# Optimization experiments

Measured on AMD Instinct MI355X. Metric: run time of the kernel, lower is better.

## Reference

```python
import jax, jax.numpy as jnp
import numpy as np

IS_CAUSAL = True
NEG_INF = float('-inf')


def setup_inputs() -> dict:
    key = jax.random.key(0)
    kq, kk, kv = jax.random.split(key, 3)
    B, H, S, D = 4, 16, 2048, 64
    return {
        'query': jax.random.normal(kq, (B, H, S, D), dtype=jnp.float32),
        'key': jax.random.normal(kk, (B, H, S, D), dtype=jnp.float32),
        'value': jax.random.normal(kv, (B, H, S, D), dtype=jnp.float32),
    }


def reference(query, key, value):
    # Attention(Q,K,V) = softmax(QK^T / sqrt(d_k) + causal_mask) V
    d_k = query.shape[-1]
    scale = 1.0 / np.sqrt(d_k).astype(np.float32)
    # [B,H,Sq,Sk]
    scores = jnp.einsum('bhqd,bhkd->bhqk', query, key) * scale
    if IS_CAUSAL:
        sq, sk = query.shape[-2], key.shape[-2]
        causal = jnp.triu(jnp.ones((sq, sk), dtype=bool), k=1)
        scores = jnp.where(causal[None, None, :, :], NEG_INF, scores)
    weights = jax.nn.softmax(scores, axis=-1)
    # dropout p=0.0 (eval): identity
    out = jnp.einsum('bhqk,bhkd->bhqd', weights, value)
    return out
```

## Files before the change

### kernel.cpp

```cpp
#include <hip/hip_runtime.h>
#include <stdint.h>


#define SLEN 2048
#define DHEAD 64
#define NHEADS 64
#define NELEM (SLEN * DHEAD * NHEADS)
#define PADP 72
#define OMPAD 68

typedef short bf16x8 __attribute__((ext_vector_type(8)));
typedef float f32x4 __attribute__((ext_vector_type(4)));

__device__ __forceinline__ uint32_t pkbf(float hi, float lo) {
    uint32_t a = __builtin_bit_cast(uint32_t, lo) + 0x8000u;
    uint32_t b = __builtin_bit_cast(uint32_t, hi) + 0x8000u;
    return __builtin_amdgcn_perm(b, a, 0x07060302u);
}
__device__ __forceinline__ unsigned short f2bf(float f) {
    return (unsigned short)((__builtin_bit_cast(uint32_t, f) + 0x8000u) >> 16);
}

__global__ __launch_bounds__(256)
void convert_prep(const float* __restrict__ K, const float* __restrict__ V,
                  unsigned short* __restrict__ Kb, unsigned short* __restrict__ Vtb) {
    __shared__ unsigned short Lt[64 * 264];
    const int b = blockIdx.x, t = threadIdx.x;
    if (b < 4096) {
        const int off = (b * 256 + t) * 8;
        float4 a = *(const float4*)(K + off);
        float4 c = *(const float4*)(K + off + 4);
        uint4 o;
        o.x = pkbf(a.y, a.x); o.y = pkbf(a.w, a.z);
        o.z = pkbf(c.y, c.x); o.w = pkbf(c.w, c.z);
        *(uint4*)(Kb + off) = o;
    } else {
        const int vb2 = b - 4096;
        const int head = vb2 >> 3, kblk = vb2 & 7;
        const float* Vh = V + (size_t)head * (SLEN * DHEAD) + kblk * 256 * DHEAD;
        unsigned short* Vo = Vtb + (size_t)head * (SLEN * DHEAD) + kblk * 256;
#pragma unroll
        for (int i = 0; i < 16; ++i) {
            int idx = t + 256 * i;
            int key = idx >> 4, d4 = idx & 15;
            float4 v = *(const float4*)(Vh + key * DHEAD + d4 * 4);
            Lt[(d4 * 4 + 0) * 264 + key] = f2bf(v.x);
            Lt[(d4 * 4 + 1) * 264 + key] = f2bf(v.y);
            Lt[(d4 * 4 + 2) * 264 + key] = f2bf(v.z);
            Lt[(d4 * 4 + 3) * 264 + key] = f2bf(v.w);
        }
        __syncthreads();
#pragma unroll
        for (int jj = 0; jj < 8; ++jj) {
            int idx = t + 256 * jj;
            int d = idx >> 5, k8 = idx & 31;
            *(uint4*)(Vo + (size_t)d * SLEN + k8 * 8) = *(const uint4*)(Lt + d * 264 + k8 * 8);
        }
    }
}

__global__ __launch_bounds__(128, 2)
void sdpa_mfma(const float* __restrict__ Qf, const unsigned short* __restrict__ Kb,
               const unsigned short* __restrict__ Vtb, float* __restrict__ Og) {
    const int n    = blockIdx.x;
    const int head = n & 63;
    const int A    = n >> 6;
    const int TB   = 31 - A;

    const size_t hb = (size_t)head * SLEN * DHEAD;
    const float* Qh = Qf + hb;
    const unsigned short* Kh  = Kb + hb;
    const unsigned short* Vth = Vtb + hb;
    float* Oh = Og + hb;

    const int tid  = threadIdx.x;
    const int w    = tid >> 6, lane = tid & 63;
    const int cl   = lane & 15, quad = lane >> 4;

    __shared__ unsigned short Pl[2 * 64 * PADP];
    __shared__ float Om[64 * OMPAD];
    __shared__ float Lsm[64];

    unsigned short* Plw = Pl + w * 64 * PADP;
    const float SCL = 0.18033688f;

    bf16x8 qf[4][2];
    bf16x8 kbn[4][2];
    f32x4  o[4][4];
    float  ls[4];

    auto load_qf = [&](int qw) {
#pragma unroll
        for (int m = 0; m < 4; ++m)
#pragma unroll
            for (int h = 0; h < 2; ++h) {
                const float* src = Qh + (size_t)(qw + m * 16 + cl) * DHEAD + h * 32 + quad * 8;
                float4 a = *(const float4*)src;
                float4 b = *(const float4*)(src + 4);
                uint4 u;
                u.x = pkbf(a.y * SCL, a.x * SCL); u.y = pkbf(a.w * SCL, a.z * SCL);
                u.z = pkbf(b.y * SCL, b.x * SCL); u.w = pkbf(b.w * SCL, b.z * SCL);
                qf[m][h] = __builtin_bit_cast(bf16x8, u);
            }
    };
    auto zero_acc = [&]() {
#pragma unroll
        for (int m = 0; m < 4; ++m) {
            ls[m] = 0.f;
#pragma unroll
            for (int d = 0; d < 4; ++d) o[m][d] = (f32x4){0.f, 0.f, 0.f, 0.f};
        }
    };
    auto load_kb = [&](int j, bf16x8 kb[4][2]) {
        const unsigned short* base = Kh + (size_t)j * 64 * DHEAD;
#pragma unroll
        for (int kk = 0; kk < 4; ++kk)
#pragma unroll
            for (int h = 0; h < 2; ++h)
                kb[kk][h] = __builtin_bit_cast(bf16x8,
                    *(const uint4*)(base + (kk * 16 + cl) * DHEAD + h * 32 + quad * 8));
    };

    auto do_steps = [&](int tq, int js, int je) {
        if (js >= je) return;
        load_kb(js, kbn);
        for (int j = js; j < je; ++j) {
            bf16x8 vb[4][2];
            const unsigned short* vbase = Vth + j * 64;
#pragma unroll
            for (int dd = 0; dd < 4; ++dd)
#pragma unroll
                for (int h = 0; h < 2; ++h)
                    vb[dd][h] = __builtin_bit_cast(bf16x8,
                        *(const uint4*)(vbase + (size_t)(dd * 16 + cl) * SLEN + h * 32 + quad * 8));

            const bool partial = (j == tq);
#pragma unroll
            for (int kk = 0; kk < 4; ++kk) {
                const int krel = kk * 16 + quad * 4;
#pragma unroll
                for (int qq = 0; qq < 4; ++qq) {
                    f32x4 s = (f32x4){0.f, 0.f, 0.f, 0.f};
                    s = __builtin_amdgcn_mfma_f32_16x16x32_bf16(kbn[kk][0], qf[qq][0], s, 0, 0, 0);
                    s = __builtin_amdgcn_mfma_f32_16x16x32_bf16(kbn[kk][1], qf[qq][1], s, 0, 0, 0);
                    float p0, p1, p2, p3;
                    if (partial) {
                        const int qrel = qq * 16 + cl;
                        p0 = (krel + 0 <= qrel) ? __builtin_amdgcn_exp2f(s[0]) : 0.f;
                        p1 = (krel + 1 <= qrel) ? __builtin_amdgcn_exp2f(s[1]) : 0.f;
                        p2 = (krel + 2 <= qrel) ? __builtin_amdgcn_exp2f(s[2]) : 0.f;
                        p3 = (krel + 3 <= qrel) ? __builtin_amdgcn_exp2f(s[3]) : 0.f;
                    } else {
                        p0 = __builtin_amdgcn_exp2f(s[0]);
                        p1 = __builtin_amdgcn_exp2f(s[1]);
                        p2 = __builtin_amdgcn_exp2f(s[2]);
                        p3 = __builtin_amdgcn_exp2f(s[3]);
                    }
                    ls[qq] += (p0 + p1) + (p2 + p3);
                    uint2 pw;
                    pw.x = pkbf(p1, p0);
                    pw.y = pkbf(p3, p2);
                    *(uint2*)(Plw + (qq * 16 + cl) * PADP + kk * 16 + quad * 4) = pw;
                }
            }
            const int jn = (j + 1 < je) ? j + 1 : j;
            load_kb(jn, kbn);

            bf16x8 pa[4][2];
#pragma unroll
            for (int m = 0; m < 4; ++m)
#pragma unroll
                for (int h = 0; h < 2; ++h)
                    pa[m][h] = __builtin_bit_cast(bf16x8,
                        *(const uint4*)(Plw + (m * 16 + cl) * PADP + h * 32 + quad * 8));
#pragma unroll
            for (int m = 0; m < 4; ++m)
#pragma unroll
                for (int dd = 0; dd < 4; ++dd) {
                    o[m][dd] = __builtin_amdgcn_mfma_f32_16x16x32_bf16(pa[m][0], vb[dd][0], o[m][dd], 0, 0, 0);
                    o[m][dd] = __builtin_amdgcn_mfma_f32_16x16x32_bf16(pa[m][1], vb[dd][1], o[m][dd], 0, 0, 0);
                }
        }
    };
    auto reduce_ls = [&]() {
#pragma unroll
        for (int qq = 0; qq < 4; ++qq) {
            float v = ls[qq];
            v += __shfl_xor(v, 16);
            v += __shfl_xor(v, 32);
            ls[qq] = v;
        }
    };
    auto store_tile = [&](int qw, const float lsr[4]) {
#pragma unroll
        for (int m = 0; m < 4; ++m)
#pragma unroll
            for (int r = 0; r < 4; ++r) {
                const float inv = 1.0f / __shfl(lsr[m], quad * 4 + r);
#pragma unroll
                for (int dd = 0; dd < 4; ++dd)
                    Oh[(size_t)(qw + m * 16 + quad * 4 + r) * DHEAD + dd * 16 + cl] = o[m][dd][r] * inv;
            }
    };

    if (w == 0) {
        load_qf(A * 64);
        zero_acc();
        do_steps(A, 0, A + 1);
        reduce_ls();
        store_tile(A * 64, ls);
        load_qf(TB * 64);
        zero_acc();
        do_steps(TB, 0, 16 - A);
        reduce_ls();
    } else {
        load_qf(TB * 64);
        zero_acc();
        do_steps(TB, 16 - A, 32 - A);
        reduce_ls();
    }

    if (w == 1) {
#pragma unroll
        for (int m = 0; m < 4; ++m)
#pragma unroll
            for (int dd = 0; dd < 4; ++dd)
                *(f32x4*)(Om + (dd * 16 + cl) * OMPAD + m * 16 + quad * 4) = o[m][dd];
        if (quad == 0) {
#pragma unroll
            for (int qq = 0; qq < 4; ++qq) Lsm[qq * 16 + cl] = ls[qq];
        }
    }
    __syncthreads();
    if (w == 0) {
#pragma unroll
        for (int m = 0; m < 4; ++m)
#pragma unroll
            for (int dd = 0; dd < 4; ++dd)
                o[m][dd] += *(const f32x4*)(Om + (dd * 16 + cl) * OMPAD + m * 16 + quad * 4);
        float lc[4];
#pragma unroll
        for (int qq = 0; qq < 4; ++qq) lc[qq] = ls[qq] + Lsm[qq * 16 + cl];
        store_tile(TB * 64, lc);
    }
}

extern "C" void kernel_launch(void* const* d_in, const int* in_sizes, int n_in,
                              void* d_out, int out_size, void* d_ws, size_t ws_size,
                              hipStream_t stream) {
    const float* Q = (const float*)d_in[0];
    const float* K = (const float*)d_in[1];
    const float* V = (const float*)d_in[2];
    float*       O = (float*)d_out;

    unsigned short* Kbf  = (unsigned short*)d_ws;
    unsigned short* Vtbf = Kbf + NELEM;

    convert_prep<<<dim3(4096 + 512), dim3(256), 0, stream>>>(K, V, Kbf, Vtbf);
    sdpa_mfma<<<dim3(1024), dim3(128), 0, stream>>>(Q, Kbf, Vtbf, O);
}
```

Before: 205.2 us.

## Shrink query tiles to 32 rows and pass P through bpermute instead of LDS

Query tiles shrink from 64 to 32 rows, so each block now runs four waves, as two pairs that each balance a light and a heavy causal tile. This raises occupancy, with launch bounds of 256 threads and 4 blocks. The probability tile is no longer written to and re-read from shared memory; it is rearranged into the MFMA A-operand layout with ds_bpermute in registers. The K-tile prefetch across iterations is dropped, and each wave now loads the same K/V for only half as many query rows, which lowers reuse per load.

```diff
diff --git a/kernel.cpp b/kernel.cpp
--- a/kernel.cpp
+++ b/kernel.cpp
@@ -6,8 +6,6 @@
 #define DHEAD 64
 #define NHEADS 64
 #define NELEM (SLEN * DHEAD * NHEADS)
-#define PADP 72
-#define OMPAD 68
 
 typedef short bf16x8 __attribute__((ext_vector_type(8)));
 typedef float f32x4 __attribute__((ext_vector_type(4)));
@@ -59,42 +57,44 @@
     }
 }
 
-__global__ __launch_bounds__(128, 2)
+__global__ __launch_bounds__(256, 4)
 void sdpa_mfma(const float* __restrict__ Qf, const unsigned short* __restrict__ Kb,
                const unsigned short* __restrict__ Vtb, float* __restrict__ Og) {
-    const int n    = blockIdx.x;
+    const int n = blockIdx.x;
     const int head = n & 63;
-    const int A    = n >> 6;
-    const int TB   = 31 - A;
+    const int cp = n >> 6;
+    const int tid = threadIdx.x;
+    const int w = tid >> 6, lane = tid & 63;
+    const int cl = lane & 15, quad = lane >> 4;
+    const int ch = w >> 1, role = w & 1;
+    const int c = cp + 16 * ch;
+    const int subA = c, subB = 63 - c;
+    const int Sa = (c >> 1) + 1;
+    const int Sb = ((63 - c) >> 1) + 1;
 
     const size_t hb = (size_t)head * SLEN * DHEAD;
     const float* Qh = Qf + hb;
-    const unsigned short* Kh  = Kb + hb;
+    const unsigned short* Kh = Kb + hb;
     const unsigned short* Vth = Vtb + hb;
     float* Oh = Og + hb;
 
-    const int tid  = threadIdx.x;
-    const int w    = tid >> 6, lane = tid & 63;
-    const int cl   = lane & 15, quad = lane >> 4;
-
-    __shared__ unsigned short Pl[2 * 64 * PADP];
-    __shared__ float Om[64 * OMPAD];
-    __shared__ float Lsm[64];
-
-    unsigned short* Plw = Pl + w * 64 * PADP;
+    __shared__ float Om[2][64 * 36];
+    __shared__ float Lsm[2][32];
+
+    const int idx0 = 4 * (cl + 32 * (quad & 1));
+    const int idx1 = idx0 + 64;
     const float SCL = 0.18033688f;
 
-    bf16x8 qf[4][2];
-    bf16x8 kbn[4][2];
-    f32x4  o[4][4];
-    float  ls[4];
-
-    auto load_qf = [&](int qw) {
-#pragma unroll
-        for (int m = 0; m < 4; ++m)
+    bf16x8 qf[2][2];
+    f32x4 o[2][4];
+    float ls[2];
+
+    auto load_qf = [&](int i) {
+#pragma unroll
+        for (int m = 0; m < 2; ++m)
 #pragma unroll
             for (int h = 0; h < 2; ++h) {
-                const float* src = Qh + (size_t)(qw + m * 16 + cl) * DHEAD + h * 32 + quad * 8;
+                const float* src = Qh + (size_t)(i * 32 + m * 16 + cl) * DHEAD + h * 32 + quad * 8;
                 float4 a = *(const float4*)src;
                 float4 b = *(const float4*)(src + 4);
                 uint4 u;
@@ -105,47 +105,45 @@
     };
     auto zero_acc = [&]() {
 #pragma unroll
-        for (int m = 0; m < 4; ++m) {
+        for (int m = 0; m < 2; ++m) {
             ls[m] = 0.f;
 #pragma unroll
             for (int d = 0; d < 4; ++d) o[m][d] = (f32x4){0.f, 0.f, 0.f, 0.f};
         }
     };
-    auto load_kb = [&](int j, bf16x8 kb[4][2]) {
-        const unsigned short* base = Kh + (size_t)j * 64 * DHEAD;
-#pragma unroll
-        for (int kk = 0; kk < 4; ++kk)
-#pragma unroll
-            for (int h = 0; h < 2; ++h)
-                kb[kk][h] = __builtin_bit_cast(bf16x8,
-                    *(const uint4*)(base + (kk * 16 + cl) * DHEAD + h * 32 + quad * 8));
-    };
-
-    auto do_steps = [&](int tq, int js, int je) {
-        if (js >= je) return;
-        load_kb(js, kbn);
+
+    auto do_steps = [&](int i, int js, int je) {
+        const int jd = i >> 1;
+        const int qrb = 32 * (i & 1);
         for (int j = js; j < je; ++j) {
-            bf16x8 vb[4][2];
+            const unsigned short* kbase = Kh + (size_t)j * 64 * DHEAD;
+            bf16x8 kb[4][2];
+#pragma unroll
+            for (int kk = 0; kk < 4; ++kk)
+#pragma unroll
+                for (int h = 0; h < 2; ++h)
+                    kb[kk][h] = __builtin_bit_cast(bf16x8,
+                        *(const uint4*)(kbase + (kk * 16 + cl) * DHEAD + h * 32 + quad * 8));
             const unsigned short* vbase = Vth + j * 64;
-#pragma unroll
-            for (int dd = 0; dd < 4; ++dd)
-#pragma unroll
-                for (int h = 0; h < 2; ++h)
-                    vb[dd][h] = __builtin_bit_cast(bf16x8,
-                        *(const uint4*)(vbase + (size_t)(dd * 16 + cl) * SLEN + h * 32 + quad * 8));
-
-            const bool partial = (j == tq);
+            bf16x8 vb0[4];
+#pragma unroll
+            for (int dd = 0; dd < 4; ++dd)
+                vb0[dd] = __builtin_bit_cast(bf16x8,
+                    *(const uint4*)(vbase + (size_t)(dd * 16 + cl) * SLEN + quad * 8));
+
+            uint32_t Sd[2][4][2];
+            const bool partial = (j == jd);
 #pragma unroll
             for (int kk = 0; kk < 4; ++kk) {
                 const int krel = kk * 16 + quad * 4;
 #pragma unroll
-                for (int qq = 0; qq < 4; ++qq) {
+                for (int qq = 0; qq < 2; ++qq) {
                     f32x4 s = (f32x4){0.f, 0.f, 0.f, 0.f};
-                    s = __builtin_amdgcn_mfma_f32_16x16x32_bf16(kbn[kk][0], qf[qq][0], s, 0, 0, 0);
-                    s = __builtin_amdgcn_mfma_f32_16x16x32_bf16(kbn[kk][1], qf[qq][1], s, 0, 0, 0);
+                    s = __builtin_amdgcn_mfma_f32_16x16x32_bf16(kb[kk][0], qf[qq][0], s, 0, 0, 0);
+                    s = __builtin_amdgcn_mfma_f32_16x16x32_bf16(kb[kk][1], qf[qq][1], s, 0, 0, 0);
                     float p0, p1, p2, p3;
                     if (partial) {
-                        const int qrel = qq * 16 + cl;
+                        const int qrel = qrb + qq * 16 + cl;
                         p0 = (krel + 0 <= qrel) ? __builtin_amdgcn_exp2f(s[0]) : 0.f;
                         p1 = (krel + 1 <= qrel) ? __builtin_amdgcn_exp2f(s[1]) : 0.f;
                         p2 = (krel + 2 <= qrel) ? __builtin_amdgcn_exp2f(s[2]) : 0.f;
@@ -157,91 +155,95 @@
                         p3 = __builtin_amdgcn_exp2f(s[3]);
                     }
                     ls[qq] += (p0 + p1) + (p2 + p3);
-                    uint2 pw;
-                    pw.x = pkbf(p1, p0);
-                    pw.y = pkbf(p3, p2);
-                    *(uint2*)(Plw + (qq * 16 + cl) * PADP + kk * 16 + quad * 4) = pw;
+                    Sd[qq][kk][0] = pkbf(p1, p0);
+                    Sd[qq][kk][1] = pkbf(p3, p2);
                 }
             }
-            const int jn = (j + 1 < je) ? j + 1 : j;
-            load_kb(jn, kbn);
-
-            bf16x8 pa[4][2];
-#pragma unroll
-            for (int m = 0; m < 4; ++m)
-#pragma unroll
-                for (int h = 0; h < 2; ++h)
-                    pa[m][h] = __builtin_bit_cast(bf16x8,
-                        *(const uint4*)(Plw + (m * 16 + cl) * PADP + h * 32 + quad * 8));
-#pragma unroll
-            for (int m = 0; m < 4; ++m)
+            bf16x8 vb1[4];
+#pragma unroll
+            for (int dd = 0; dd < 4; ++dd)
+                vb1[dd] = __builtin_bit_cast(bf16x8,
+                    *(const uint4*)(vbase + (size_t)(dd * 16 + cl) * SLEN + 32 + quad * 8));
+
+            bf16x8 pa[2][2];
+#pragma unroll
+            for (int qq = 0; qq < 2; ++qq)
+#pragma unroll
+                for (int h = 0; h < 2; ++h) {
+                    uint32_t dw[4];
+#pragma unroll
+                    for (int dp = 0; dp < 4; ++dp) {
+                        const int id = (dp < 2) ? idx0 : idx1;
+                        int ra = __builtin_amdgcn_ds_bpermute(id, (int)Sd[qq][2 * h][dp & 1]);
+                        int rb = __builtin_amdgcn_ds_bpermute(id, (int)Sd[qq][2 * h + 1][dp & 1]);
+                        dw[dp] = (quad < 2) ? (uint32_t)ra : (uint32_t)rb;
+                    }
+                    uint4 u; u.x = dw[0]; u.y = dw[1]; u.z = dw[2]; u.w = dw[3];
+                    pa[qq][h] = __builtin_bit_cast(bf16x8, u);
+                }
+#pragma unroll
+            for (int m = 0; m < 2; ++m)
 #pragma unroll
                 for (int dd = 0; dd < 4; ++dd) {
-                    o[m][dd] = __builtin_amdgcn_mfma_f32_16x16x32_bf16(pa[m][0], vb[dd][0], o[m][dd], 0, 0, 0);
-                    o[m][dd] = __builtin_amdgcn_mfma_f32_16x16x32_bf16(pa[m][1], vb[dd][1], o[m][dd], 0, 0, 0);
+                    o[m][dd] = __builtin_amdgcn_mfma_f32_16x16x32_bf16(pa[m][0], vb0[dd], o[m][dd], 0, 0, 0);
+                    o[m][dd] = __builtin_amdgcn_mfma_f32_16x16x32_bf16(pa[m][1], vb1[dd], o[m][dd], 0, 0, 0);
                 }
         }
     };
     auto reduce_ls = [&]() {
 #pragma unroll
-        for (int qq = 0; qq < 4; ++qq) {
+        for (int qq = 0; qq < 2; ++qq) {
             float v = ls[qq];
             v += __shfl_xor(v, 16);
             v += __shfl_xor(v, 32);
             ls[qq] = v;
         }
     };
-    auto store_tile = [&](int qw, const float lsr[4]) {
-#pragma unroll
-        for (int m = 0; m < 4; ++m)
+    auto store_tile = [&](int i, const float* lsr) {
+#pragma unroll
+        for (int m = 0; m < 2; ++m)
 #pragma unroll
             for (int r = 0; r < 4; ++r) {
                 const float inv = 1.0f / __shfl(lsr[m], quad * 4 + r);
 #pragma unroll
                 for (int dd = 0; dd < 4; ++dd)
-                    Oh[(size_t)(qw + m * 16 + quad * 4 + r) * DHEAD + dd * 16 + cl] = o[m][dd][r] * inv;
+                    Oh[(size_t)(i * 32 + m * 16 + quad * 4 + r) * DHEAD + dd * 16 + cl] = o[m][dd][r] * inv;
             }
     };
 
-    if (w == 0) {
-        load_qf(A * 64);
-        zero_acc();
-        do_steps(A, 0, A + 1);
+    if (role == 0) {
+        load_qf(subA); zero_acc();
+        do_steps(subA, 0, Sa);
         reduce_ls();
-        store_tile(A * 64, ls);
-        load_qf(TB * 64);
-        zero_acc();
-        do_steps(TB, 0, 16 - A);
+        store_tile(subA, ls);
+        load_qf(subB); zero_acc();
+        do_steps(subB, 0, Sb - 16);
         reduce_ls();
     } else {
-        load_qf(TB * 64);
-        zero_acc();
-        do_steps(TB, 16 - A, 32 - A);
+        load_qf(subB); zero_acc();
+        do_steps(subB, Sb - 16, Sb);
         reduce_ls();
-    }
-
-    if (w == 1) {
-#pragma unroll
-        for (int m = 0; m < 4; ++m)
-#pragma unroll
-            for (int dd = 0; dd < 4; ++dd)
-                *(f32x4*)(Om + (dd * 16 + cl) * OMPAD + m * 16 + quad * 4) = o[m][dd];
+#pragma unroll
+        for (int m = 0; m < 2; ++m)
+#pragma unroll
+            for (int dd = 0; dd < 4; ++dd)
+                *(f32x4*)&Om[ch][(dd * 16 + cl) * 36 + m * 16 + quad * 4] = o[m][dd];
         if (quad == 0) {
 #pragma unroll
-            for (int qq = 0; qq < 4; ++qq) Lsm[qq * 16 + cl] = ls[qq];
+            for (int qq = 0; qq < 2; ++qq) Lsm[ch][qq * 16 + cl] = ls[qq];
         }
     }
     __syncthreads();
-    if (w == 0) {
-#pragma unroll
-        for (int m = 0; m < 4; ++m)
-#pragma unroll
-            for (int dd = 0; dd < 4; ++dd)
-                o[m][dd] += *(const f32x4*)(Om + (dd * 16 + cl) * OMPAD + m * 16 + quad * 4);
-        float lc[4];
-#pragma unroll
-        for (int qq = 0; qq < 4; ++qq) lc[qq] = ls[qq] + Lsm[qq * 16 + cl];
-        store_tile(TB * 64, lc);
+    if (role == 0) {
+#pragma unroll
+        for (int m = 0; m < 2; ++m)
+#pragma unroll
+            for (int dd = 0; dd < 4; ++dd)
+                o[m][dd] += *(const f32x4*)&Om[ch][(dd * 16 + cl) * 36 + m * 16 + quad * 4];
+        float lc[2];
+#pragma unroll
+        for (int qq = 0; qq < 2; ++qq) lc[qq] = ls[qq] + Lsm[ch][qq * 16 + cl];
+        store_tile(subB, lc);
     }
 }
 
@@ -257,5 +259,5 @@
     unsigned short* Vtbf = Kbf + NELEM;
 
     convert_prep<<<dim3(4096 + 512), dim3(256), 0, stream>>>(K, V, Kbf, Vtbf);
-    sdpa_mfma<<<dim3(1024), dim3(128), 0, stream>>>(Q, Kbf, Vtbf, O);
-}
+    sdpa_mfma<<<dim3(1024), dim3(256), 0, stream>>>(Q, Kbf, Vtbf, O);
+}
```

Result: slower. 269.7 us (+31.4%).
